# Performance work log

Measured on AMD Instinct MI355X. Metric: run time of the kernel, lower is better.

Reference implementation:

```python
import jax, jax.numpy as jnp
import numpy as np
import math

B, T, E, H = 4, 1024, 1024, 16
HD = E // H  # 64, even -> rope_dim == head_dim, no pass-through
SCALE = HD ** -0.5
PI = math.pi


def setup_inputs() -> dict:
    key = jax.random.key(0)
    ks = jax.random.split(key, 16)
    d = {}
    d["x_real"] = jax.random.normal(ks[0], (B, T, E), jnp.float32)
    d["x_imag"] = jax.random.normal(ks[1], (B, T, E), jnp.float32)
    d["lat"] = jax.random.uniform(ks[2], (B, T), jnp.float32) * 180.0
    d["lon"] = jax.random.uniform(ks[3], (B, T), jnp.float32) * 360.0
    i = 4
    for p in ("q", "k", "v", "o"):
        d[p + "_log_mag"] = jax.random.normal(ks[i], (E, E), jnp.float32) * 0.1; i += 1
        d[p + "_phase"] = jax.random.uniform(ks[i], (E, E), jnp.float32, minval=-PI, maxval=PI); i += 1
        d[p + "_bmag"] = jnp.zeros((E,), jnp.float32)
        d[p + "_bphase"] = jnp.zeros((E,), jnp.float32)
    d["dist_scale"] = jax.random.normal(ks[i], (H,), jnp.float32) * 0.1 - 0.5; i += 1
    d["dist_offset"] = jnp.zeros((H,), jnp.float32)
    return d


def _clinear(xr, xi, log_mag, phase, bmag, bphase):
    # Complex linear with magnitude-phase weights: W = exp(log_mag) * e^{i*phase}
    mag = jnp.exp(log_mag)
    wr = mag * jnp.cos(phase)
    wi = mag * jnp.sin(phase)
    r = xr @ wr.T - xi @ wi.T + bmag * jnp.cos(bphase)
    im = xr @ wi.T + xi @ wr.T + bmag * jnp.sin(bphase)
    return r, im


def _rotate_half(x):
    x1, x2 = jnp.split(x, 2, axis=-1)
    return jnp.concatenate([-x2, x1], axis=-1)


def _rope(xr, xi, cos_full, sin_full):
    # applied identically to real and imag parts (head_dim even -> full rope)
    r = xr * cos_full + _rotate_half(xr) * sin_full
    im = xi * cos_full + _rotate_half(xi) * sin_full
    return r, im


def _heads(x):  # [B,T,E] -> [B,H,T,HD]
    return x.reshape(B, T, H, HD).transpose(0, 2, 1, 3)


def _forward(x_real, x_imag, lat, lon,
             q_log_mag, q_phase, q_bmag, q_bphase,
             k_log_mag, k_phase, k_bmag, k_bphase,
             v_log_mag, v_phase, v_bmag, v_bphase,
             o_log_mag, o_phase, o_bmag, o_bphase,
             dist_scale, dist_offset):
    qr, qi = _clinear(x_real, x_imag, q_log_mag, q_phase, q_bmag, q_bphase)
    kr, ki = _clinear(x_real, x_imag, k_log_mag, k_phase, k_bmag, k_bphase)
    vr, vi = _clinear(x_real, x_imag, v_log_mag, v_phase, v_bmag, v_bphase)
    qr, qi, kr, ki, vr, vi = map(_heads, (qr, qi, kr, ki, vr, vi))

    # complex RoPE cache
    pos = jnp.arange(T, dtype=jnp.float32)
    inv_freq = 1.0 / (10000.0 ** (jnp.arange(0, HD, 2, dtype=jnp.float32) / HD))
    freqs = pos[:, None] * inv_freq[None, :]          # [T, HD/2]
    cos = jnp.cos(freqs); sin = jnp.sin(freqs)
    cos_full = jnp.concatenate([cos, cos], -1)[None, None]  # [1,1,T,HD]
    sin_full = jnp.concatenate([sin, sin], -1)[None, None]
    qr, qi = _rope(qr, qi, cos_full, sin_full)
    kr, ki = _rope(kr, ki, cos_full, sin_full)

    # Hermitian attention scores: Re(Q K^H) = Re(Q)Re(K)^T + Im(Q)Im(K)^T
    scores = (jnp.einsum('bhqd,bhkd->bhqk', qr, kr)
              + jnp.einsum('bhqd,bhkd->bhqk', qi, ki)) * SCALE

    # spatial attention bias via haversine distance
    lat_rad = (lat - 90.0) / 180.0 * PI
    lon_rad = lon / 360.0 * (2.0 * PI)
    lat1 = lat_rad[:, :, None]; lat2 = lat_rad[:, None, :]   # [B,T,1],[B,1,T]
    dlat = lat2 - lat1
    dlon = lon_rad[:, None, :] - lon_rad[:, :, None]
    a = jnp.sin(dlat / 2) ** 2 + jnp.cos(lat1) * jnp.cos(lat2) * jnp.sin(dlon / 2) ** 2
    dist_deg = 2.0 * jnp.arcsin(jnp.sqrt(jnp.clip(a, 0.0, 1.0))) * (180.0 / PI)
    log_dist = jnp.log1p(dist_deg)[:, None]                  # [B,1,T,T]
    bias = dist_scale[None, :, None, None] * log_dist + dist_offset[None, :, None, None]
    scores = scores + bias

    # causal mask (block_size == T)
    causal = jnp.tril(jnp.ones((T, T), dtype=bool))
    scores = jnp.where(causal[None, None], scores, jnp.float32(-1e9))
    attn = jax.nn.softmax(scores, axis=-1)

    # complex value aggregation: real attention weights times complex V
    or_ = jnp.einsum('bhqk,bhkd->bhqd', attn, vr)
    oi_ = jnp.einsum('bhqk,bhkd->bhqd', attn, vi)
    or_ = or_.transpose(0, 2, 1, 3).reshape(B, T, E)
    oi_ = oi_.transpose(0, 2, 1, 3).reshape(B, T, E)

    yr, yi = _clinear(or_, oi_, o_log_mag, o_phase, o_bmag, o_bphase)
    return jnp.stack([yr, yi])  # [2,B,T,E] (real, imag)


def reference(x_real, x_imag, lat, lon,
              q_log_mag, q_phase, q_bmag, q_bphase,
              k_log_mag, k_phase, k_bmag, k_bphase,
              v_log_mag, v_phase, v_bmag, v_bphase,
              o_log_mag, o_phase, o_bmag, o_bphase,
              dist_scale, dist_offset):
    return _forward(x_real, x_imag, lat, lon,
                    q_log_mag, q_phase, q_bmag, q_bphase,
                    k_log_mag, k_phase, k_bmag, k_bphase,
                    v_log_mag, v_phase, v_bmag, v_bphase,
                    o_log_mag, o_phase, o_bmag, o_bphase,
                    dist_scale, dist_offset)
```

## Files before the change

kernel.cpp:

```cpp
#include <hip/hip_runtime.h>
#include <math.h>

#define B_ 4
#define T_ 1024
#define E_ 1024
#define H_ 16
#define HD_ 64

constexpr float SCALE_ = 0.125f;
constexpr float PI_F = 3.14159265358979323846f;

constexpr size_t BTE = (size_t)B_ * T_ * E_;
constexpr size_t BTT = (size_t)B_ * T_ * T_;
constexpr int M_ = B_ * T_;
constexpr int KC_ = 2 * E_;

typedef __attribute__((ext_vector_type(8))) short bf16x8;
typedef __attribute__((ext_vector_type(4))) float f32x4;

__device__ __forceinline__ short f2bf(float f) {
    unsigned int u = __float_as_uint(f);
    unsigned int r = (u + 0x7fffu + ((u >> 16) & 1u)) >> 16;
    return (short)r;
}
__device__ __forceinline__ float bf2f(short s) {
    return __uint_as_float(((unsigned int)(unsigned short)s) << 16);
}
__device__ __forceinline__ void fsplit(float v, short& h, short& l) {
    short hh = f2bf(v);
    h = hh;
    l = f2bf(v - bf2f(hh));
}
__device__ __forceinline__ void gl_lds16(const void* g, void* l) {
    __builtin_amdgcn_global_load_lds(
        (const __attribute__((address_space(1))) unsigned int*)g,
        (__attribute__((address_space(3))) unsigned int*)l, 16, 0, 0);
}

__global__ __launch_bounds__(256) void wgen(const float* __restrict__ lm,
                                            const float* __restrict__ ph,
                                            short* __restrict__ W) {
    int idx = blockIdx.x * 256 + threadIdx.x;
    int n = idx >> 10, k = idx & 1023;
    float m = expf(lm[idx]);
    float s, c;
    sincosf(ph[idx], &s, &c);
    float wr = m * c, wi = m * s;
    size_t r0 = (size_t)n * KC_;
    size_t r1 = (size_t)(n + 1024) * KC_;
    W[r0 + k]        = f2bf(wr);
    W[r0 + 1024 + k] = f2bf(-wi);
    W[r1 + k]        = f2bf(wi);
    W[r1 + 1024 + k] = f2bf(wr);
}

__global__ __launch_bounds__(256) void wgen_split(const float* __restrict__ lm,
                                                  const float* __restrict__ ph,
                                                  short* __restrict__ Wh,
                                                  short* __restrict__ Wl) {
    int idx = blockIdx.x * 256 + threadIdx.x;
    int n = idx >> 10, k = idx & 1023;
    float m = expf(lm[idx]);
    float s, c;
    sincosf(ph[idx], &s, &c);
    float wr = m * c, wi = m * s;
    size_t o0 = (size_t)n * KC_ + k;
    size_t o1 = (size_t)n * KC_ + 1024 + k;
    size_t o2 = (size_t)(n + 1024) * KC_ + k;
    size_t o3 = (size_t)(n + 1024) * KC_ + 1024 + k;
    short h, l;
    fsplit(wr,  h, l); Wh[o0] = h; Wl[o0] = l;
    fsplit(-wi, h, l); Wh[o1] = h; Wl[o1] = l;
    fsplit(wi,  h, l); Wh[o2] = h; Wl[o2] = l;
    fsplit(wr,  h, l); Wh[o3] = h; Wl[o3] = l;
}

__global__ __launch_bounds__(256) void xcat_split(const float* __restrict__ xr,
                                                  const float* __restrict__ xi,
                                                  short* __restrict__ xh,
                                                  short* __restrict__ xl) {
    size_t idx = (size_t)blockIdx.x * 256 + threadIdx.x;
    size_t m = idx >> 10, k = idx & 1023;
    short h, l;
    fsplit(xr[idx], h, l);
    xh[m * KC_ + k] = h; xl[m * KC_ + k] = l;
    fsplit(xi[idx], h, l);
    xh[m * KC_ + 1024 + k] = h; xl[m * KC_ + 1024 + k] = l;
}

__global__ __launch_bounds__(256) void geodist(const float* __restrict__ lat,
                                               const float* __restrict__ lon,
                                               short* __restrict__ ld) {
    size_t idx = (size_t)blockIdx.x * 256 + threadIdx.x;
    int k = (int)(idx & (T_ - 1));
    int q = (int)((idx >> 10) & (T_ - 1));
    int b = (int)(idx >> 20);
    float la1 = (lat[b * T_ + q] - 90.f) * (PI_F / 180.f);
    float la2 = (lat[b * T_ + k] - 90.f) * (PI_F / 180.f);
    float lo1 = lon[b * T_ + q] * (PI_F / 180.f);
    float lo2 = lon[b * T_ + k] * (PI_F / 180.f);
    float sdla = sinf((la2 - la1) * 0.5f);
    float sdlo = sinf((lo2 - lo1) * 0.5f);
    float a = sdla * sdla + cosf(la1) * cosf(la2) * sdlo * sdlo;
    a = fminf(fmaxf(a, 0.f), 1.f);
    float dd = 2.f * asinf(sqrtf(a)) * (180.f / PI_F);
    ld[idx] = f2bf(log1pf(dd));
}

__global__ __launch_bounds__(256) void cgemm_qk2(const short* __restrict__ Ah,
                                                 const short* __restrict__ Al,
                                                 const short* __restrict__ Qwh,
                                                 const short* __restrict__ Qwl,
                                                 const short* __restrict__ Kwh,
                                                 const short* __restrict__ Kwl,
                                                 const float* __restrict__ qbm,
                                                 const float* __restrict__ qbp,
                                                 const float* __restrict__ kbm,
                                                 const float* __restrict__ kbp,
                                                 short* __restrict__ Qh,
                                                 short* __restrict__ Ql,
                                                 short* __restrict__ Kh,
                                                 short* __restrict__ Kl) {
    __shared__ short sA[128 * 64];
    __shared__ short sQ[128 * 64];
    __shared__ short sK[128 * 64];

    const int tid = threadIdx.x;
    const int w = tid >> 6, l = tid & 63;
    const int wm = w >> 1, wn = w & 1;
    const int wl = l & 15, g = l >> 4;

    int id = blockIdx.y * 32 + blockIdx.x;
    int swz = (id & 7) * 64 + (id >> 3);
    const int bm = (swz & 31) * 128;
    const int bn = (swz >> 5) * 128;

    f32x4 accQ[4][4], accK[4][4];
#pragma unroll
    for (int m = 0; m < 4; ++m)
#pragma unroll
        for (int n = 0; n < 4; ++n) {
            accQ[m][n] = (f32x4){0.f, 0.f, 0.f, 0.f};
            accK[m][n] = (f32x4){0.f, 0.f, 0.f, 0.f};
        }

    for (int k0 = 0; k0 < KC_; k0 += 32) {
        __syncthreads();
#pragma unroll
        for (int i = 0; i < 4; ++i) {
            const int chunk = (w * 4 + i) * 64 + l;
            const int row = chunk >> 3;
            const int c8 = (chunk & 7) ^ (row & 7);
            const size_t ca = (size_t)(bm + row) * KC_ + k0 + (c8 & 3) * 8;
            const size_t cb = (size_t)(bn + row) * KC_ + k0 + (c8 & 3) * 8;
            gl_lds16(((c8 < 4) ? Ah : Al) + ca, sA + (size_t)(w * 4 + i) * 64 * 8);
            gl_lds16(((c8 < 4) ? Qwh : Qwl) + cb, sQ + (size_t)(w * 4 + i) * 64 * 8);
            gl_lds16(((c8 < 4) ? Kwh : Kwl) + cb, sK + (size_t)(w * 4 + i) * 64 * 8);
        }
        __syncthreads();

        bf16x8 afh[4], afl[4];
#pragma unroll
        for (int m = 0; m < 4; ++m) {
            const int ra = wm * 64 + m * 16 + wl;
            const int sw = ra & 7;
            afh[m] = *(const bf16x8*)&sA[(ra * 8 + (g ^ sw)) * 8];
            afl[m] = *(const bf16x8*)&sA[(ra * 8 + ((g + 4) ^ sw)) * 8];
        }
#pragma unroll
        for (int n = 0; n < 4; ++n) {
            const int rb = wn * 64 + n * 16 + wl;
            const int sw = rb & 7;
            const bf16x8 qh_ = *(const bf16x8*)&sQ[(rb * 8 + (g ^ sw)) * 8];
            const bf16x8 ql_ = *(const bf16x8*)&sQ[(rb * 8 + ((g + 4) ^ sw)) * 8];
            const bf16x8 kh_ = *(const bf16x8*)&sK[(rb * 8 + (g ^ sw)) * 8];
            const bf16x8 kl_ = *(const bf16x8*)&sK[(rb * 8 + ((g + 4) ^ sw)) * 8];
#pragma unroll
            for (int m = 0; m < 4; ++m) {
                accQ[m][n] = __builtin_amdgcn_mfma_f32_16x16x32_bf16(afh[m], qh_, accQ[m][n], 0, 0, 0);
                accQ[m][n] = __builtin_amdgcn_mfma_f32_16x16x32_bf16(afh[m], ql_, accQ[m][n], 0, 0, 0);
                accQ[m][n] = __builtin_amdgcn_mfma_f32_16x16x32_bf16(afl[m], qh_, accQ[m][n], 0, 0, 0);
                accK[m][n] = __builtin_amdgcn_mfma_f32_16x16x32_bf16(afh[m], kh_, accK[m][n], 0, 0, 0);
                accK[m][n] = __builtin_amdgcn_mfma_f32_16x16x32_bf16(afh[m], kl_, accK[m][n], 0, 0, 0);
                accK[m][n] = __builtin_amdgcn_mfma_f32_16x16x32_bf16(afl[m], kh_, accK[m][n], 0, 0, 0);
            }
        }
    }

#pragma unroll
    for (int n = 0; n < 4; ++n) {
        const int col = bn + wn * 64 + n * 16 + wl;
        const int ch = col & 1023;
        float qs, qc, ks, kc;
        sincosf(qbp[ch], &qs, &qc);
        sincosf(kbp[ch], &ks, &kc);
        const float qbias = qbm[ch] * (col < 1024 ? qc : qs);
        const float kbias = kbm[ch] * (col < 1024 ? kc : ks);
#pragma unroll
        for (int m = 0; m < 4; ++m)
#pragma unroll
            for (int r = 0; r < 4; ++r) {
                accQ[m][n][r] += qbias;
                accK[m][n][r] += kbias;
            }
    }

#pragma unroll
    for (int n = 0; n < 2; ++n) {
        const int j = n * 16 + wl;
        const float invf = expf(-(2.f * j / 64.f) * 9.210340371976184f);
#pragma unroll
        for (int m = 0; m < 4; ++m)
#pragma unroll
            for (int r = 0; r < 4; ++r) {
                const int row = bm + wm * 64 + m * 16 + g * 4 + r;
                const float th = (float)(row & 1023) * invf;
                float s_, c_;
                sincosf(th, &s_, &c_);
                float x1 = accQ[m][n][r], x2 = accQ[m][n + 2][r];
                accQ[m][n][r]     = x1 * c_ - x2 * s_;
                accQ[m][n + 2][r] = x2 * c_ + x1 * s_;
                x1 = accK[m][n][r]; x2 = accK[m][n + 2][r];
                accK[m][n][r]     = x1 * c_ - x2 * s_;
                accK[m][n + 2][r] = x2 * c_ + x1 * s_;
            }
    }

#pragma unroll
    for (int n = 0; n < 4; ++n) {
        const int col = bn + wn * 64 + n * 16 + wl;
        const int ch = col & 1023;
        const int off = (ch >> 6) * 128 + (ch & 63) + ((col >= 1024) ? 64 : 0);
#pragma unroll
        for (int m = 0; m < 4; ++m)
#pragma unroll
            for (int r = 0; r < 4; ++r) {
                const int row = bm + wm * 64 + m * 16 + g * 4 + r;
                short h_, l_;
                fsplit(accQ[m][n][r], h_, l_);
                Qh[(size_t)row * KC_ + off] = h_;
                Ql[(size_t)row * KC_ + off] = l_;
                fsplit(accK[m][n][r], h_, l_);
                Kh[(size_t)row * KC_ + off] = h_;
                Kl[(size_t)row * KC_ + off] = l_;
            }
    }
}

__global__ __launch_bounds__(256) void cgemm_mfma(const short* __restrict__ A,
                                                  const short* __restrict__ W,
                                                  const float* __restrict__ bmag,
                                                  const float* __restrict__ bphase,
                                                  short* __restrict__ outbf,
                                                  float* __restrict__ outr,
                                                  float* __restrict__ outi,
                                                  int mode) {
    __shared__ short sAB[128 * 64];

    const int tid = threadIdx.x;
    const int w = tid >> 6, l = tid & 63;
    const int wm = w >> 1, wn = w & 1;
    const int wl = l & 15, g = l >> 4;

    int id = blockIdx.y * 32 + blockIdx.x;
    int swz = (id & 7) * 64 + (id >> 3);
    const int bm = (swz & 31) * 128;
    const int bn = (swz >> 5) * 128;

    f32x4 acc[4][4];
#pragma unroll
    for (int m = 0; m < 4; ++m)
#pragma unroll
        for (int n = 0; n < 4; ++n) acc[m][n] = (f32x4){0.f, 0.f, 0.f, 0.f};

    for (int k0 = 0; k0 < KC_; k0 += 32) {
        __syncthreads();
#pragma unroll
        for (int i = 0; i < 4; ++i) {
            const int chunk = (w * 4 + i) * 64 + l;
            const int row = chunk >> 3;
            const int c8 = (chunk & 7) ^ (row & 7);
            const short* src = (c8 < 4)
                ? A + (size_t)(bm + row) * KC_ + k0 + (c8 & 3) * 8
                : W + (size_t)(bn + row) * KC_ + k0 + (c8 & 3) * 8;
            gl_lds16(src, sAB + (size_t)(w * 4 + i) * 64 * 8);
        }
        __syncthreads();

        bf16x8 af[4], bfr[4];
#pragma unroll
        for (int m = 0; m < 4; ++m) {
            const int ra = wm * 64 + m * 16 + wl;
            af[m] = *(const bf16x8*)&sAB[(ra * 8 + (g ^ (ra & 7))) * 8];
        }
#pragma unroll
        for (int n = 0; n < 4; ++n) {
            const int rb = wn * 64 + n * 16 + wl;
            bfr[n] = *(const bf16x8*)&sAB[(rb * 8 + ((g + 4) ^ (rb & 7))) * 8];
        }
#pragma unroll
        for (int m = 0; m < 4; ++m)
#pragma unroll
            for (int n = 0; n < 4; ++n)
                acc[m][n] = __builtin_amdgcn_mfma_f32_16x16x32_bf16(af[m], bfr[n], acc[m][n], 0, 0, 0);
    }

#pragma unroll
    for (int n = 0; n < 4; ++n) {
        const int col = bn + wn * 64 + n * 16 + wl;
        const int ch = col & 1023;
        float sb, cb;
        sincosf(bphase[ch], &sb, &cb);
        const float bias = bmag[ch] * (col < 1024 ? cb : sb);
#pragma unroll
        for (int m = 0; m < 4; ++m) {
#pragma unroll
            for (int r = 0; r < 4; ++r) {
                const int row = bm + wm * 64 + m * 16 + g * 4 + r;
                const float v = acc[m][n][r] + bias;
                if (mode == 0) {
                    const int hh = ch >> 6, d = ch & 63;
                    outbf[(size_t)row * KC_ + hh * 128 + d + ((col >= 1024) ? 64 : 0)] = f2bf(v);
                } else {
                    if (col < 1024) outr[(size_t)row * E_ + col] = v;
                    else            outi[(size_t)row * E_ + (col - 1024)] = v;
                }
            }
        }
    }
}

__global__ __launch_bounds__(512) void attn_split(const short* __restrict__ qh,
                                                  const short* __restrict__ ql,
                                                  const short* __restrict__ kh,
                                                  const short* __restrict__ kl,
                                                  const short* __restrict__ vc,
                                                  const short* __restrict__ ldb,
                                                  const float* __restrict__ dsc,
                                                  const float* __restrict__ dof,
                                                  short* __restrict__ otc) {
    __shared__ short sKh[64 * 128];
    __shared__ short sKl[64 * 128];
    __shared__ short sV[2][64 * 66];
    __shared__ short sP[8][16 * 68];

    const int j = blockIdx.x;
    const int h = j & 15;
    const int idx = j >> 4;
    const int b = idx & 3;
    const int q4 = idx >> 2;
    const int qt = (q4 < 4) ? (7 - q4) : (q4 - 4);

    const int tid = threadIdx.x;
    const int w = tid >> 6, l = tid & 63;
    const int wl = l & 15, g = l >> 4;

    const float dsch = dsc[h], dofh = dof[h];

    bf16x8 aqh[4], aql[4];
    {
        const size_t qbase = ((size_t)(b * T_) + qt * 128 + w * 16 + wl) * KC_ + h * 128;
#pragma unroll
        for (int ks = 0; ks < 4; ++ks) {
            aqh[ks] = *(const bf16x8*)(qh + qbase + ks * 32 + g * 8);
            aql[ks] = *(const bf16x8*)(ql + qbase + ks * 32 + g * 8);
        }
    }

    f32x4 accR[4], accI[4];
#pragma unroll
    for (int nb = 0; nb < 4; ++nb) {
        accR[nb] = (f32x4){0.f, 0.f, 0.f, 0.f};
        accI[nb] = (f32x4){0.f, 0.f, 0.f, 0.f};
    }
    float m_run[4], l_run[4];
#pragma unroll
    for (int r = 0; r < 4; ++r) { m_run[r] = -3.0e38f; l_run[r] = 0.f; }

    const int nkt = 2 * qt + 2;
    for (int kt = 0; kt < nkt; ++kt) {
        __syncthreads();

#pragma unroll
        for (int i = 0; i < 2; ++i) {
            int chunk = (w * 2 + i) * 64 + l;
            int row = chunk >> 4;
            int c8 = (chunk & 15) ^ (row & 15);
            size_t src = ((size_t)(b * T_) + kt * 64 + row) * KC_ + h * 128 + c8 * 8;
            gl_lds16(kh + src, sKh + (w * 2 + i) * 64 * 8);
            gl_lds16(kl + src, sKl + (w * 2 + i) * 64 * 8);
        }
        {
            const short* vrow = vc + ((size_t)(b * T_) + kt * 64 + l) * KC_ + h * 128;
            const int comp = w >> 2;
            const int d0 = (w & 3) * 16;
#pragma unroll
            for (int half = 0; half < 2; ++half) {
                bf16x8 v8 = *(const bf16x8*)(vrow + comp * 64 + d0 + half * 8);
#pragma unroll
                for (int jj = 0; jj < 8; ++jj) sV[comp][(d0 + half * 8 + jj) * 66 + l] = v8[jj];
            }
        }
        __syncthreads();

        f32x4 s[4];
#pragma unroll
        for (int nb = 0; nb < 4; ++nb) s[nb] = (f32x4){0.f, 0.f, 0.f, 0.f};
#pragma unroll
        for (int nb = 0; nb < 4; ++nb) {
            const int ktl = nb * 16 + wl;
#pragma unroll
            for (int ks = 0; ks < 4; ++ks) {
                const int pc8 = (ks * 4 + g) ^ (ktl & 15);
                const bf16x8 bkh = *(const bf16x8*)&sKh[ktl * 128 + pc8 * 8];
                const bf16x8 bkl = *(const bf16x8*)&sKl[ktl * 128 + pc8 * 8];
                s[nb] = __builtin_amdgcn_mfma_f32_16x16x32_bf16(aqh[ks], bkh, s[nb], 0, 0, 0);
                s[nb] = __builtin_amdgcn_mfma_f32_16x16x32_bf16(aqh[ks], bkl, s[nb], 0, 0, 0);
                s[nb] = __builtin_amdgcn_mfma_f32_16x16x32_bf16(aql[ks], bkh, s[nb], 0, 0, 0);
            }
        }

        const int qg0 = qt * 128 + w * 16 + g * 4;
        const int kg0 = kt * 64;
        const bool domask = (kt >= 2 * qt);
#pragma unroll
        for (int nb = 0; nb < 4; ++nb) {
            const int kg = kg0 + nb * 16 + wl;
            const short* ldp = ldb + ((size_t)b * T_ + qg0) * T_ + kg;
#pragma unroll
            for (int r = 0; r < 4; ++r) {
                float sv = s[nb][r] * SCALE_ + dsch * bf2f(ldp[(size_t)r * T_]) + dofh;
                if (domask && kg > qg0 + r) sv = -1.0e9f;
                s[nb][r] = sv;
            }
        }

#pragma unroll
        for (int r = 0; r < 4; ++r) {
            float mt = fmaxf(fmaxf(s[0][r], s[1][r]), fmaxf(s[2][r], s[3][r]));
            mt = fmaxf(mt, __shfl_xor(mt, 1));
            mt = fmaxf(mt, __shfl_xor(mt, 2));
            mt = fmaxf(mt, __shfl_xor(mt, 4));
            mt = fmaxf(mt, __shfl_xor(mt, 8));
            const float mnew = fmaxf(m_run[r], mt);
            const float sc = __expf(m_run[r] - mnew);
            m_run[r] = mnew;
            float rs = 0.f;
#pragma unroll
            for (int nb = 0; nb < 4; ++nb) {
                const float p = __expf(s[nb][r] - mnew);
                s[nb][r] = p;
                rs += p;
            }
            rs += __shfl_xor(rs, 1);
            rs += __shfl_xor(rs, 2);
            rs += __shfl_xor(rs, 4);
            rs += __shfl_xor(rs, 8);
            l_run[r] = l_run[r] * sc + rs;
#pragma unroll
            for (int nb = 0; nb < 4; ++nb) { accR[nb][r] *= sc; accI[nb][r] *= sc; }
        }

#pragma unroll
        for (int nb = 0; nb < 4; ++nb)
#pragma unroll
            for (int r = 0; r < 4; ++r)
                sP[w][(g * 4 + r) * 68 + nb * 16 + wl] = f2bf(s[nb][r]);

        bf16x8 ap[2];
#pragma unroll
        for (int ks = 0; ks < 2; ++ks)
            ap[ks] = *(const bf16x8*)&sP[w][wl * 68 + ks * 32 + g * 8];
#pragma unroll
        for (int nb = 0; nb < 4; ++nb) {
#pragma unroll
            for (int ks = 0; ks < 2; ++ks) {
                const bf16x8 bvr = *(const bf16x8*)&sV[0][(nb * 16 + wl) * 66 + ks * 32 + g * 8];
                const bf16x8 bvi = *(const bf16x8*)&sV[1][(nb * 16 + wl) * 66 + ks * 32 + g * 8];
                accR[nb] = __builtin_amdgcn_mfma_f32_16x16x32_bf16(ap[ks], bvr, accR[nb], 0, 0, 0);
                accI[nb] = __builtin_amdgcn_mfma_f32_16x16x32_bf16(ap[ks], bvi, accI[nb], 0, 0, 0);
            }
        }
    }

    float inv[4];
#pragma unroll
    for (int r = 0; r < 4; ++r) inv[r] = 1.0f / l_run[r];
#pragma unroll
    for (int nb = 0; nb < 4; ++nb) {
#pragma unroll
        for (int r = 0; r < 4; ++r) {
            const int q = qt * 128 + w * 16 + g * 4 + r;
            const int d = nb * 16 + wl;
            const size_t base = ((size_t)(b * T_) + q) * KC_ + h * 64 + d;
            otc[base] = f2bf(accR[nb][r] * inv[r]);
            otc[base + 1024] = f2bf(accI[nb][r] * inv[r]);
        }
    }
}

extern "C" void kernel_launch(void* const* d_in, const int* in_sizes, int n_in,
                              void* d_out, int out_size, void* d_ws, size_t ws_size,
                              hipStream_t stream) {
    const float* x_r  = (const float*)d_in[0];
    const float* x_i  = (const float*)d_in[1];
    const float* lat  = (const float*)d_in[2];
    const float* lon  = (const float*)d_in[3];
    const float* q_lm = (const float*)d_in[4];
    const float* q_ph = (const float*)d_in[5];
    const float* q_bm = (const float*)d_in[6];
    const float* q_bp = (const float*)d_in[7];
    const float* k_lm = (const float*)d_in[8];
    const float* k_ph = (const float*)d_in[9];
    const float* k_bm = (const float*)d_in[10];
    const float* k_bp = (const float*)d_in[11];
    const float* v_lm = (const float*)d_in[12];
    const float* v_ph = (const float*)d_in[13];
    const float* v_bm = (const float*)d_in[14];
    const float* v_bp = (const float*)d_in[15];
    const float* o_lm = (const float*)d_in[16];
    const float* o_ph = (const float*)d_in[17];
    const float* o_bm = (const float*)d_in[18];
    const float* o_bp = (const float*)d_in[19];
    const float* dsc  = (const float*)d_in[20];
    const float* dof  = (const float*)d_in[21];

    char* ws = (char*)d_ws;
    const size_t MB = 1024u * 1024u;
    short* Wv  = (short*)(ws + 0 * MB);
    short* Wo  = (short*)(ws + 8 * MB);
    short* Wqh = (short*)(ws + 16 * MB);
    short* Wql = (short*)(ws + 24 * MB);
    short* Wkh = (short*)(ws + 32 * MB);
    short* Wkl = (short*)(ws + 40 * MB);
    short* xch = (short*)(ws + 48 * MB);
    short* xcl = (short*)(ws + 64 * MB);
    short* qhh = (short*)(ws + 80 * MB);
    short* qll = (short*)(ws + 96 * MB);
    short* khh = (short*)(ws + 112 * MB);
    short* kll = (short*)(ws + 128 * MB);
    short* vcb = (short*)(ws + 144 * MB);
    short* otc = (short*)(ws + 160 * MB);
    short* ldt = (short*)(ws + 176 * MB);

    wgen_split<<<(E_ * E_) / 256, 256, 0, stream>>>(q_lm, q_ph, Wqh, Wql);
    wgen_split<<<(E_ * E_) / 256, 256, 0, stream>>>(k_lm, k_ph, Wkh, Wkl);
    wgen<<<(E_ * E_) / 256, 256, 0, stream>>>(v_lm, v_ph, Wv);
    wgen<<<(E_ * E_) / 256, 256, 0, stream>>>(o_lm, o_ph, Wo);
    xcat_split<<<BTE / 256, 256, 0, stream>>>(x_r, x_i, xch, xcl);
    geodist<<<BTT / 256, 256, 0, stream>>>(lat, lon, ldt);

    dim3 ggrid(M_ / 128, KC_ / 128);
    cgemm_qk2<<<ggrid, 256, 0, stream>>>(xch, xcl, Wqh, Wql, Wkh, Wkl,
                                         q_bm, q_bp, k_bm, k_bp,
                                         qhh, qll, khh, kll);
    cgemm_mfma<<<ggrid, 256, 0, stream>>>(xch, Wv, v_bm, v_bp, vcb, nullptr, nullptr, 0);

    attn_split<<<512, 512, 0, stream>>>(qhh, qll, khh, kll, vcb, ldt, dsc, dof, otc);

    float* yr = (float*)d_out;
    float* yi = (float*)d_out + BTE;
    cgemm_mfma<<<ggrid, 256, 0, stream>>>(otc, Wo, o_bm, o_bp, nullptr, yr, yi, 1);
}
```

Measured before the change: 601.8 us.

## Double-buffer LDS in GEMM kernels and enlarge QK GEMM tile to 256 rows

Result: no change. 603.6 us (+0.3%).

```diff
diff --git a/kernel.cpp b/kernel.cpp
--- a/kernel.cpp
+++ b/kernel.cpp
@@ -107,33 +107,33 @@
     ld[idx] = f2bf(log1pf(dd));
 }
 
-__global__ __launch_bounds__(256) void cgemm_qk2(const short* __restrict__ Ah,
-                                                 const short* __restrict__ Al,
-                                                 const short* __restrict__ Qwh,
-                                                 const short* __restrict__ Qwl,
-                                                 const short* __restrict__ Kwh,
-                                                 const short* __restrict__ Kwl,
-                                                 const float* __restrict__ qbm,
-                                                 const float* __restrict__ qbp,
-                                                 const float* __restrict__ kbm,
-                                                 const float* __restrict__ kbp,
-                                                 short* __restrict__ Qh,
-                                                 short* __restrict__ Ql,
-                                                 short* __restrict__ Kh,
-                                                 short* __restrict__ Kl) {
-    __shared__ short sA[128 * 64];
-    __shared__ short sQ[128 * 64];
-    __shared__ short sK[128 * 64];
+__global__ __launch_bounds__(512, 2) void cgemm_qk2(const short* __restrict__ Ah,
+                                                    const short* __restrict__ Al,
+                                                    const short* __restrict__ Qwh,
+                                                    const short* __restrict__ Qwl,
+                                                    const short* __restrict__ Kwh,
+                                                    const short* __restrict__ Kwl,
+                                                    const float* __restrict__ qbm,
+                                                    const float* __restrict__ qbp,
+                                                    const float* __restrict__ kbm,
+                                                    const float* __restrict__ kbp,
+                                                    short* __restrict__ Qh,
+                                                    short* __restrict__ Ql,
+                                                    short* __restrict__ Kh,
+                                                    short* __restrict__ Kl) {
+    __shared__ short lds[2][4096 * 8];
 
     const int tid = threadIdx.x;
     const int w = tid >> 6, l = tid & 63;
-    const int wm = w >> 1, wn = w & 1;
+    const int wm = w >> 1;
+    const int wn = w & 1;
     const int wl = l & 15, g = l >> 4;
 
-    int id = blockIdx.y * 32 + blockIdx.x;
-    int swz = (id & 7) * 64 + (id >> 3);
-    const int bm = (swz & 31) * 128;
-    const int bn = (swz >> 5) * 128;
+    const int id = blockIdx.x;
+    const int x = id & 7;
+    const int j = id >> 3;
+    const int bm = ((x & 3) * 4 + (j & 3)) * 256;
+    const int bnc = ((x >> 2) * 8 + (j >> 2)) * 128;
 
     f32x4 accQ[4][4], accK[4][4];
 #pragma unroll
@@ -144,20 +144,35 @@
             accK[m][n] = (f32x4){0.f, 0.f, 0.f, 0.f};
         }
 
-    for (int k0 = 0; k0 < KC_; k0 += 32) {
-        __syncthreads();
-#pragma unroll
-        for (int i = 0; i < 4; ++i) {
-            const int chunk = (w * 4 + i) * 64 + l;
-            const int row = chunk >> 3;
-            const int c8 = (chunk & 7) ^ (row & 7);
-            const size_t ca = (size_t)(bm + row) * KC_ + k0 + (c8 & 3) * 8;
-            const size_t cb = (size_t)(bn + row) * KC_ + k0 + (c8 & 3) * 8;
-            gl_lds16(((c8 < 4) ? Ah : Al) + ca, sA + (size_t)(w * 4 + i) * 64 * 8);
-            gl_lds16(((c8 < 4) ? Qwh : Qwl) + cb, sQ + (size_t)(w * 4 + i) * 64 * 8);
-            gl_lds16(((c8 < 4) ? Kwh : Kwl) + cb, sK + (size_t)(w * 4 + i) * 64 * 8);
-        }
-        __syncthreads();
+    auto stage = [&](int k0, int buf) {
+#pragma unroll
+        for (int i = 0; i < 8; ++i) {
+            const int c = i * 512 + tid;
+            short* dst = &lds[buf][(size_t)c * 8];
+            if (c < 2048) {
+                const int row = c >> 3, c8 = (c & 7) ^ (row & 7);
+                gl_lds16(((c8 < 4) ? Ah : Al) + (size_t)(bm + row) * KC_ + k0 + (c8 & 3) * 8, dst);
+            } else if (c < 3072) {
+                const int lc = c - 2048, row = lc >> 3, c8 = (lc & 7) ^ (row & 7);
+                gl_lds16(((c8 < 4) ? Qwh : Qwl) + (size_t)(bnc + row) * KC_ + k0 + (c8 & 3) * 8, dst);
+            } else {
+                const int lc = c - 3072, row = lc >> 3, c8 = (lc & 7) ^ (row & 7);
+                gl_lds16(((c8 < 4) ? Kwh : Kwl) + (size_t)(bnc + row) * KC_ + k0 + (c8 & 3) * 8, dst);
+            }
+        }
+    };
+
+    const int NT = KC_ / 32;
+    stage(0, 0);
+    __syncthreads();
+
+    int cur = 0;
+    for (int t = 0; t < NT; ++t) {
+        if (t + 1 < NT) stage((t + 1) * 32, cur ^ 1);
+
+        const short* sA = &lds[cur][0];
+        const short* sQ = &lds[cur][2048 * 8];
+        const short* sK = &lds[cur][3072 * 8];
 
         bf16x8 afh[4], afl[4];
 #pragma unroll
@@ -185,11 +200,13 @@
                 accK[m][n] = __builtin_amdgcn_mfma_f32_16x16x32_bf16(afl[m], kh_, accK[m][n], 0, 0, 0);
             }
         }
+        __syncthreads();
+        cur ^= 1;
     }
 
 #pragma unroll
     for (int n = 0; n < 4; ++n) {
-        const int col = bn + wn * 64 + n * 16 + wl;
+        const int col = bnc + wn * 64 + n * 16 + wl;
         const int ch = col & 1023;
         float qs, qc, ks, kc;
         sincosf(qbp[ch], &qs, &qc);
@@ -207,8 +224,8 @@
 
 #pragma unroll
     for (int n = 0; n < 2; ++n) {
-        const int j = n * 16 + wl;
-        const float invf = expf(-(2.f * j / 64.f) * 9.210340371976184f);
+        const int jf = n * 16 + wl;
+        const float invf = expf(-(2.f * jf / 64.f) * 9.210340371976184f);
 #pragma unroll
         for (int m = 0; m < 4; ++m)
 #pragma unroll
@@ -228,7 +245,7 @@
 
 #pragma unroll
     for (int n = 0; n < 4; ++n) {
-        const int col = bn + wn * 64 + n * 16 + wl;
+        const int col = bnc + wn * 64 + n * 16 + wl;
         const int ch = col & 1023;
         const int off = (ch >> 6) * 128 + (ch & 63) + ((col >= 1024) ? 64 : 0);
 #pragma unroll
@@ -255,7 +272,7 @@
                                                   float* __restrict__ outr,
                                                   float* __restrict__ outi,
                                                   int mode) {
-    __shared__ short sAB[128 * 64];
+    __shared__ short lds[2][1024 * 8];
 
     const int tid = threadIdx.x;
     const int w = tid >> 6, l = tid & 63;
@@ -273,20 +290,27 @@
 #pragma unroll
         for (int n = 0; n < 4; ++n) acc[m][n] = (f32x4){0.f, 0.f, 0.f, 0.f};
 
-    for (int k0 = 0; k0 < KC_; k0 += 32) {
-        __syncthreads();
+    auto stage = [&](int k0, int buf) {
 #pragma unroll
         for (int i = 0; i < 4; ++i) {
-            const int chunk = (w * 4 + i) * 64 + l;
-            const int row = chunk >> 3;
-            const int c8 = (chunk & 7) ^ (row & 7);
+            const int c = i * 256 + tid;
+            const int row = c >> 3, c8 = (c & 7) ^ (row & 7);
             const short* src = (c8 < 4)
                 ? A + (size_t)(bm + row) * KC_ + k0 + (c8 & 3) * 8
                 : W + (size_t)(bn + row) * KC_ + k0 + (c8 & 3) * 8;
-            gl_lds16(src, sAB + (size_t)(w * 4 + i) * 64 * 8);
-        }
-        __syncthreads();
-
+            gl_lds16(src, &lds[buf][(size_t)c * 8]);
+        }
+    };
+
+    const int NT = KC_ / 32;
+    stage(0, 0);
+    __syncthreads();
+
+    int cur = 0;
+    for (int t = 0; t < NT; ++t) {
+        if (t + 1 < NT) stage((t + 1) * 32, cur ^ 1);
+
+        const short* sAB = lds[cur];
         bf16x8 af[4], bfr[4];
 #pragma unroll
         for (int m = 0; m < 4; ++m) {
@@ -303,6 +327,9 @@
 #pragma unroll
             for (int n = 0; n < 4; ++n)
                 acc[m][n] = __builtin_amdgcn_mfma_f32_16x16x32_bf16(af[m], bfr[n], acc[m][n], 0, 0, 0);
+
+        __syncthreads();
+        cur ^= 1;
     }
 
 #pragma unroll
@@ -550,10 +577,11 @@
     xcat_split<<<BTE / 256, 256, 0, stream>>>(x_r, x_i, xch, xcl);
     geodist<<<BTT / 256, 256, 0, stream>>>(lat, lon, ldt);
 
+    cgemm_qk2<<<256, 512, 0, stream>>>(xch, xcl, Wqh, Wql, Wkh, Wkl,
+                                       q_bm, q_bp, k_bm, k_bp,
+                                       qhh, qll, khh, kll);
+
     dim3 ggrid(M_ / 128, KC_ / 128);
-    cgemm_qk2<<<ggrid, 256, 0, stream>>>(xch, xcl, Wqh, Wql, Wkh, Wkl,
-                                         q_bm, q_bp, k_bm, k_bp,
-                                         qhh, qll, khh, kll);
     cgemm_mfma<<<ggrid, 256, 0, stream>>>(xch, Wv, v_bm, v_bp, vcb, nullptr, nullptr, 0);
 
     attn_split<<<512, 512, 0, stream>>>(qhh, qll, khh, kll, vcb, ldt, dsc, dof, otc);
```
